# Kernel tuning notes

Measured on AMD Instinct MI355X. Metric: run time of the kernel, lower is better.

## Reference

```python
import jax, jax.numpy as jnp
import numpy as np

B, SQ, SK, D, H, F = 8, 512, 1024, 1024, 16, 4096
DK = D // H
NEG_INF = -jnp.inf


def _linear(x, w, b):
    return x @ w + b


def _mha(q, k, v, wq, bq, wk, bk, wv, bv, wo, bo, causal, kv_mask):
    # q: [B,Sq,D], k/v: [B,Sk,D]
    b, sq, d = q.shape
    sk = k.shape[1]
    Q = _linear(q, wq, bq).reshape(b, sq, H, DK).transpose(0, 2, 1, 3)  # [B,H,Sq,dk]
    K = _linear(k, wk, bk).reshape(b, sk, H, DK).transpose(0, 2, 1, 3)
    V = _linear(v, wv, bv).reshape(b, sk, H, DK).transpose(0, 2, 1, 3)
    S = jnp.einsum('bhqd,bhkd->bhqk', Q, K) / jnp.sqrt(jnp.asarray(DK, Q.dtype))
    if kv_mask is not None:
        S = jnp.where(kv_mask[:, None, None, :] == 0, NEG_INF, S)
    if causal:
        tri = jnp.tril(jnp.ones((sq, sk), dtype=bool))
        S = jnp.where(tri, S, NEG_INF)
    A = jax.nn.softmax(S, axis=-1)  # dropout p=0 -> identity
    x = jnp.einsum('bhqk,bhkd->bhqd', A, V).transpose(0, 2, 1, 3).reshape(b, sq, d)
    return _linear(x, wo, bo), A


def _ln(x, g, beta, eps=1e-5):
    mu = jnp.mean(x, axis=-1, keepdims=True)
    var = jnp.mean(jnp.square(x - mu), axis=-1, keepdims=True)
    return (x - mu) * jax.lax.rsqrt(var + eps) * g + beta


def setup_inputs() -> dict:
    key = jax.random.key(0)
    ks = jax.random.split(key, 32)
    s = 0.02
    inp = {
        'x': jax.random.normal(ks[0], (B, SQ, D), jnp.float32),
        'enc_o': jax.random.normal(ks[1], (B, SK, D), jnp.float32),
        'enc_mask': jax.random.randint(ks[2], (B, SK), 0, 2, jnp.int32),
    }
    i = 3
    for pfx in ('a1', 'a2'):
        for nm in ('wq', 'wk', 'wv', 'wo'):
            inp[f'{pfx}_{nm}'] = jax.random.normal(ks[i], (D, D), jnp.float32) * s; i += 1
            inp[f'{pfx}_{nm[1:] and "b" + nm[1:]}'] = jnp.zeros((D,), jnp.float32)
    inp['ff_w1'] = jax.random.normal(ks[i], (D, F), jnp.float32) * s; i += 1
    inp['ff_b1'] = jnp.zeros((F,), jnp.float32)
    inp['ff_w2'] = jax.random.normal(ks[i], (F, D), jnp.float32) * s; i += 1
    inp['ff_b2'] = jnp.zeros((D,), jnp.float32)
    for n in ('ln1', 'ln2', 'ln3'):
        inp[f'{n}_g'] = jnp.ones((D,), jnp.float32)
        inp[f'{n}_b'] = jnp.zeros((D,), jnp.float32)
    return inp


def reference(x, enc_o, enc_mask,
              a1_wq, a1_bq, a1_wk, a1_bk, a1_wv, a1_bv, a1_wo, a1_bo,
              a2_wq, a2_bq, a2_wk, a2_bk, a2_wv, a2_bv, a2_wo, a2_bo,
              ff_w1, ff_b1, ff_w2, ff_b2,
              ln1_g, ln1_b, ln2_g, ln2_b, ln3_g, ln3_b):
    res, _ = _mha(x, x, x, a1_wq, a1_bq, a1_wk, a1_bk, a1_wv, a1_bv, a1_wo, a1_bo,
                  causal=True, kv_mask=None)
    x = _ln(x + res, ln1_g, ln1_b)
    res, attn = _mha(x, enc_o, enc_o, a2_wq, a2_bq, a2_wk, a2_bk, a2_wv, a2_bv, a2_wo, a2_bo,
                     causal=False, kv_mask=enc_mask)
    x = _ln(x + res, ln2_g, ln2_b)
    res = _linear(jax.nn.relu(_linear(x, ff_w1, ff_b1)), ff_w2, ff_b2)
    x = _ln(x + res, ln3_g, ln3_b)
    return (x, attn)
```

## Files before the change

### kernel.cpp

```cpp
#include <hip/hip_runtime.h>
#include <hip/hip_bf16.h>


using bf16 = __hip_bfloat16;
typedef __attribute__((ext_vector_type(8))) short short8;
typedef __attribute__((ext_vector_type(4))) float f32x4;

#define DEVINL __device__ __forceinline__

DEVINL unsigned short bf16bits(float f) {
  __hip_bfloat16 h = __float2bfloat16(f);
  return *reinterpret_cast<unsigned short*>(&h);
}
DEVINL float bits2f(unsigned short u) {
  return __uint_as_float(((unsigned int)u) << 16);
}
DEVINL float tofloat(float f) { return f; }
DEVINL float tofloat(bf16 h) { return __bfloat162float(h); }

#define GLD16(gp, lp) __builtin_amdgcn_global_load_lds( \
    (__attribute__((address_space(1))) const void*)(gp), \
    (__attribute__((address_space(3))) void*)(lp), 16, 0, 0)

struct GemmP {
  const bf16* A; const bf16* Bt; void* C;
  const float* bias; const int* kmask;
  float scale;
  int M, N, K, lda, ldb, ldc;
  long sAb, sAh, sBb, sBh, sCb, sCh;
};

enum { EPI_BIAS_BF16 = 0, EPI_CAUSAL_BF16, EPI_KMASK_F32, EPI_NONE_BF16,
       EPI_BIAS_F32, EPI_BIAS_RELU_BF16, EPI_PART_F32 };

template<int EPI>
DEVINL void gemm_body(const GemmP& p, int bx, int by, int bz) {
  __shared__ bf16 As[128 * 32];
  __shared__ bf16 Bs[128 * 32];
  const int t = threadIdx.x;
  const int lane = t & 63;
  const int w = t >> 6;
  const int zb = bz >> 4, zh = bz & 15;
  const int m0 = by * 128, n0 = bx * 128;

  const bf16* Ab = p.A + (long)zb * p.sAb + (long)zh * p.sAh;
  const bf16* Bb = p.Bt + (long)zb * p.sBb + (long)zh * p.sBh;
  const int fl = lane & 15, fq = lane >> 4;
  const int wm = (w >> 1) * 64, wn = (w & 1) * 64;

  f32x4 acc[4][4];
#pragma unroll
  for (int i = 0; i < 4; ++i)
#pragma unroll
    for (int j = 0; j < 4; ++j) acc[i][j] = (f32x4){0.f, 0.f, 0.f, 0.f};

  const int sr = t >> 2;
  const int sc = (t & 3) * 8;
  char* ldsA = (char*)As + w * 1024;
  char* ldsB = (char*)Bs + w * 1024;

  int brow0 = n0 + sr;      if (brow0 > p.N - 1) brow0 = p.N - 1;
  int brow1 = n0 + sr + 64; if (brow1 > p.N - 1) brow1 = p.N - 1;

  for (int k0 = 0; k0 < p.K; k0 += 32) {
    GLD16(Ab + (long)(m0 + sr) * p.lda + k0 + sc, ldsA);
    GLD16(Ab + (long)(m0 + sr + 64) * p.lda + k0 + sc, ldsA + 4096);
    GLD16(Bb + (long)brow0 * p.ldb + k0 + sc, ldsB);
    GLD16(Bb + (long)brow1 * p.ldb + k0 + sc, ldsB + 4096);
    __syncthreads();

    short8 af[4], bfv[4];
#pragma unroll
    for (int i = 0; i < 4; ++i)
      af[i] = *(const short8*)(As + (wm + i * 16 + fl) * 32 + fq * 8);
#pragma unroll
    for (int j = 0; j < 4; ++j)
      bfv[j] = *(const short8*)(Bs + (wn + j * 16 + fl) * 32 + fq * 8);
#pragma unroll
    for (int i = 0; i < 4; ++i)
#pragma unroll
      for (int j = 0; j < 4; ++j)
        acc[i][j] = __builtin_amdgcn_mfma_f32_16x16x32_bf16(af[i], bfv[j], acc[i][j], 0, 0, 0);
    __syncthreads();
  }

  const float NEGINF = -__builtin_inff();
  const long cbase = (long)zb * p.sCb + (long)zh * p.sCh;
#pragma unroll
  for (int i = 0; i < 4; ++i) {
#pragma unroll
    for (int j = 0; j < 4; ++j) {
#pragma unroll
      for (int r = 0; r < 4; ++r) {
        int row = m0 + wm + i * 16 + fq * 4 + r;
        int col = n0 + wn + j * 16 + fl;
        if (col < p.N) {
          float v = acc[i][j][r];
          if (EPI == EPI_BIAS_BF16 || EPI == EPI_BIAS_F32 || EPI == EPI_BIAS_RELU_BF16)
            v += p.bias[col];
          if (EPI == EPI_BIAS_RELU_BF16) v = v > 0.f ? v : 0.f;
          if (EPI == EPI_CAUSAL_BF16) { v *= p.scale; if (col > row) v = NEGINF; }
          if (EPI == EPI_KMASK_F32)   { v *= p.scale; if (p.kmask[zb * 1024 + col] == 0) v = NEGINF; }
          long off = cbase + (long)row * p.ldc + col;
          if (EPI == EPI_KMASK_F32 || EPI == EPI_BIAS_F32 || EPI == EPI_PART_F32)
            ((float*)p.C)[off] = v;
          else ((bf16*)p.C)[off] = __float2bfloat16(v);
        }
      }
    }
  }
}

template<int EPI>
__global__ __launch_bounds__(256)
void gemm_k(GemmP p) {
  gemm_body<EPI>(p, blockIdx.x, blockIdx.y, blockIdx.z);
}

struct Gemm2P { GemmP a, b; int nA, axw, bxw; };
__global__ __launch_bounds__(256)
void gemm2_k(Gemm2P q) {
  const int b = blockIdx.x;
  if (b < q.nA) gemm_body<EPI_BIAS_BF16>(q.a, b % q.axw, b / q.axw, 0);
  else { const int c = b - q.nA; gemm_body<EPI_BIAS_BF16>(q.b, c % q.bxw, c / q.bxw, 0); }
}

struct AttnP {
  const bf16 *Q, *K, *Vt;
  float* Pout; bf16* O;
  const int* kmask;
  int ldq, ldk, ldv;
  long sQb, sQh, sKb, sKh, sVb, sVh, sPb, sPh, sOb, sOh;
};

template<int SK, bool CAUSAL, bool WRITE_P>
__global__ __launch_bounds__(512)
void attn_fused_k(AttnP p) {
  constexpr int TKMAX = SK / 64;
  __shared__ bf16 S[64 * SK];
  __shared__ bf16 ring[3 * 4096];
  const int t = threadIdx.x;
  const int lane = t & 63;
  const int w = t >> 6;
  const int fl = lane & 15, fq = lane >> 4;
  const int qh = w >> 2;
  const int wc = w & 3;
  const int lin = blockIdx.x;
  const int wg = (lin & 7) * 128 + (lin >> 3);
  const int by = wg & 7;
  const int z = wg >> 3;
  const int zb = z >> 4, zh = z & 15;
  const int q0 = by * 64;
  const float NEGINF = -__builtin_inff();

  const bf16* Qb = p.Q + (long)zb * p.sQb + (long)zh * p.sQh;
  const bf16* Kb = p.K + (long)zb * p.sKb + (long)zh * p.sKh;
  const bf16* Vb = p.Vt + (long)zb * p.sVb + (long)zh * p.sVh;

  const int Tk = CAUSAL ? (q0 >> 6) + 1 : TKMAX;

  short8 af[2][2];
#pragma unroll
  for (int i = 0; i < 2; ++i)
#pragma unroll
    for (int kk = 0; kk < 2; ++kk)
      af[i][kk] = *(const short8*)(Qb + (long)(q0 + qh * 32 + i * 16 + fl) * p.ldq + kk * 32 + fq * 8);

  int kmv[CAUSAL ? 1 : TKMAX];
  if (!CAUSAL) {
#pragma unroll
    for (int kt = 0; kt < TKMAX; ++kt)
      kmv[kt] = p.kmask[zb * 1024 + kt * 64 + wc * 16 + fl];
  }

  const int so = t * 16;
  const int srow = so >> 7;
  const int scb = (so & 127) ^ ((srow & 7) << 4);
  auto stage = [&](const bf16* mb, int ld, int roff, int coff, int buf) {
    GLD16(mb + (long)(roff + srow) * ld + coff + (scb >> 1),
          (char*)ring + buf * 8192 + w * 1024);
  };

  stage(Kb, p.ldk, 0, 0, 0);
  if (Tk > 1) stage(Kb, p.ldk, 64, 0, 1);
  for (int kt = 0; kt < Tk; ++kt) {
    if (kt + 1 < Tk) asm volatile("s_waitcnt vmcnt(1)" ::: "memory");
    else             asm volatile("s_waitcnt vmcnt(0)" ::: "memory");
    __builtin_amdgcn_s_barrier();
    if (kt + 2 < Tk) stage(Kb, p.ldk, (kt + 2) * 64, 0, (kt + 2) % 3);

    const char* kb = (const char*)ring + (kt % 3) * 8192;
    const int krow = wc * 16 + fl;
    short8 bfv[2];
#pragma unroll
    for (int kk = 0; kk < 2; ++kk)
      bfv[kk] = *(const short8*)(kb + ((krow * 128 + kk * 64 + fq * 16) ^ ((krow & 7) << 4)));
    f32x4 acc[2] = {(f32x4){0.f,0.f,0.f,0.f}, (f32x4){0.f,0.f,0.f,0.f}};
#pragma unroll
    for (int kk = 0; kk < 2; ++kk) {
      acc[0] = __builtin_amdgcn_mfma_f32_16x16x32_bf16(af[0][kk], bfv[kk], acc[0], 0, 0, 0);
      acc[1] = __builtin_amdgcn_mfma_f32_16x16x32_bf16(af[1][kk], bfv[kk], acc[1], 0, 0, 0);
    }
    const int col = kt * 64 + krow;
    const bool mok = CAUSAL || (kmv[CAUSAL ? 0 : kt] != 0);
#pragma unroll
    for (int i = 0; i < 2; ++i) {
#pragma unroll
      for (int r = 0; r < 4; ++r) {
        int row = qh * 32 + i * 16 + fq * 4 + r;
        float v = acc[i][r] * 0.125f;
        if (CAUSAL) { if (col > q0 + row) v = NEGINF; }
        else if (!mok) v = NEGINF;
        *(bf16*)((char*)S + (((row * SK + col) * 2) ^ ((row & 7) << 4))) = __float2bfloat16(v);
      }
    }
  }
  asm volatile("s_waitcnt lgkmcnt(0)" ::: "memory");
  __builtin_amdgcn_s_barrier();

  const int Tv = Tk;
  stage(Vb, p.ldv, 0, 0, 0);
  if (Tv > 1) stage(Vb, p.ldv, 0, 64, 1);

  float* Pf = WRITE_P ? (p.Pout + (long)zb * p.sPb + (long)zh * p.sPh) : nullptr;
  constexpr int NC = SK / 512;
  const int lim = Tk * 64;
  for (int rr = 0; rr < 8; ++rr) {
    const int row = w * 8 + rr;
    const int rg = q0 + row;
    const int swz = (row & 7) << 4;
    float fv[NC][8];
#pragma unroll
    for (int c = 0; c < NC; ++c) {
      const int col = c * 512 + lane * 8;
      if (!CAUSAL || col < lim) {
        short8 sv = *(const short8*)((char*)S + (((row * SK + col) * 2) ^ swz));
#pragma unroll
        for (int j = 0; j < 8; ++j) fv[c][j] = bits2f((unsigned short)sv[j]);
      } else {
#pragma unroll
        for (int j = 0; j < 8; ++j) fv[c][j] = NEGINF;
      }
    }
    float mx = fv[0][0];
#pragma unroll
    for (int c = 0; c < NC; ++c)
#pragma unroll
      for (int j = 0; j < 8; ++j) mx = fmaxf(mx, fv[c][j]);
    for (int off = 32; off; off >>= 1) mx = fmaxf(mx, __shfl_xor(mx, off, 64));
    float s = 0.f;
#pragma unroll
    for (int c = 0; c < NC; ++c)
#pragma unroll
      for (int j = 0; j < 8; ++j) { fv[c][j] = expf(fv[c][j] - mx); s += fv[c][j]; }
    for (int off = 32; off; off >>= 1) s += __shfl_xor(s, off, 64);
    const float inv = 1.f / s;
#pragma unroll
    for (int c = 0; c < NC; ++c) {
      const int col = c * 512 + lane * 8;
      if (!CAUSAL || col < lim) {
        short8 o;
#pragma unroll
        for (int j = 0; j < 8; ++j) o[j] = (short)bf16bits(fv[c][j] * inv);
        *(short8*)((char*)S + (((row * SK + col) * 2) ^ swz)) = o;
        if (WRITE_P) {
          float* pp = Pf + (long)rg * SK + col;
          f32x4 o0, o1;
#pragma unroll
          for (int j = 0; j < 4; ++j) { o0[j] = fv[c][j] * inv; o1[j] = fv[c][4 + j] * inv; }
          *(f32x4*)pp = o0;
          *(f32x4*)(pp + 4) = o1;
        }
      }
    }
  }
  asm volatile("s_waitcnt lgkmcnt(0)" ::: "memory");
  __builtin_amdgcn_s_barrier();

  f32x4 ao[2] = {(f32x4){0.f,0.f,0.f,0.f}, (f32x4){0.f,0.f,0.f,0.f}};
  for (int vt = 0; vt < Tv; ++vt) {
    if (vt + 1 < Tv) asm volatile("s_waitcnt vmcnt(1)" ::: "memory");
    else             asm volatile("s_waitcnt vmcnt(0)" ::: "memory");
    __builtin_amdgcn_s_barrier();
    if (vt + 2 < Tv) stage(Vb, p.ldv, 0, (vt + 2) * 64, (vt + 2) % 3);

    const char* vbuf = (const char*)ring + (vt % 3) * 8192;
    const int vrow = wc * 16 + fl;
    short8 bv[2];
#pragma unroll
    for (int kk = 0; kk < 2; ++kk)
      bv[kk] = *(const short8*)(vbuf + ((vrow * 128 + kk * 64 + fq * 16) ^ ((vrow & 7) << 4)));
#pragma unroll
    for (int i = 0; i < 2; ++i) {
      const int row = qh * 32 + i * 16 + fl;
#pragma unroll
      for (int kk = 0; kk < 2; ++kk) {
        const int col = vt * 64 + kk * 32 + fq * 8;
        short8 pa = *(const short8*)((char*)S + (((row * SK + col) * 2) ^ ((row & 7) << 4)));
        ao[i] = __builtin_amdgcn_mfma_f32_16x16x32_bf16(pa, bv[kk], ao[i], 0, 0, 0);
      }
    }
  }

  bf16* Ob_ = p.O + (long)zb * p.sOb + (long)zh * p.sOh;
#pragma unroll
  for (int i = 0; i < 2; ++i)
#pragma unroll
    for (int r = 0; r < 4; ++r) {
      int row = q0 + qh * 32 + i * 16 + fq * 4 + r;
      Ob_[(long)row * 1024 + wc * 16 + fl] = __float2bfloat16(ao[i][r]);
    }
}

template<int NP>
__global__ __launch_bounds__(256)
void ln_fuse_k(const float* __restrict__ x, const float* __restrict__ part, long pstride,
               const float* __restrict__ pb,
               const float* __restrict__ g, const float* __restrict__ bt,
               float* __restrict__ outf, bf16* __restrict__ outb) {
  const int lane = threadIdx.x & 63;
  const long row = (long)blockIdx.x * 4 + (threadIdx.x >> 6);
  const float* px = x + row * 1024;
  float4 v[4];
  float s = 0.f;
#pragma unroll
  for (int c = 0; c < 4; ++c) {
    const int col = c * 256 + lane * 4;
    float4 a = *(const float4*)(px + col);
    float4 bb = *(const float4*)(pb + col);
    v[c].x = a.x + bb.x; v[c].y = a.y + bb.y; v[c].z = a.z + bb.z; v[c].w = a.w + bb.w;
#pragma unroll
    for (int sl = 0; sl < NP; ++sl) {
      float4 pp = *(const float4*)(part + sl * pstride + row * 1024 + col);
      v[c].x += pp.x; v[c].y += pp.y; v[c].z += pp.z; v[c].w += pp.w;
    }
    s += v[c].x + v[c].y + v[c].z + v[c].w;
  }
  for (int off = 32; off; off >>= 1) s += __shfl_xor(s, off, 64);
  float mu = s * (1.f / 1024.f);
  float q = 0.f;
#pragma unroll
  for (int c = 0; c < 4; ++c) {
    float dx = v[c].x - mu, dy = v[c].y - mu, dz = v[c].z - mu, dw = v[c].w - mu;
    q += dx * dx + dy * dy + dz * dz + dw * dw;
  }
  for (int off = 32; off; off >>= 1) q += __shfl_xor(q, off, 64);
  float rs = rsqrtf(q * (1.f / 1024.f) + 1e-5f);
#pragma unroll
  for (int c = 0; c < 4; ++c) {
    int col = c * 256 + lane * 4;
    float4 gg = *(const float4*)(g + col);
    float4 bb = *(const float4*)(bt + col);
    float4 o;
    o.x = (v[c].x - mu) * rs * gg.x + bb.x;
    o.y = (v[c].y - mu) * rs * gg.y + bb.y;
    o.z = (v[c].z - mu) * rs * gg.z + bb.z;
    o.w = (v[c].w - mu) * rs * gg.w + bb.w;
    *(float4*)(outf + row * 1024 + col) = o;
    if (outb) {
      uint2 pk;
      pk.x = bf16bits(o.x) | ((unsigned)bf16bits(o.y) << 16);
      pk.y = bf16bits(o.z) | ((unsigned)bf16bits(o.w) << 16);
      *(uint2*)(outb + row * 1024 + col) = pk;
    }
  }
}

template<typename TI>
DEVINL void tr_body(const TI* __restrict__ pin, bf16* __restrict__ pout,
                    int ldi, int ldo, int c0, int r0, int t, float tile[32][33]) {
  const int tx = t & 31, ty = t >> 5;
#pragma unroll
  for (int i = 0; i < 32; i += 8)
    tile[ty + i][tx] = tofloat(pin[(long)(r0 + ty + i) * ldi + c0 + tx]);
  __syncthreads();
#pragma unroll
  for (int i = 0; i < 32; i += 8)
    pout[(long)(c0 + ty + i) * ldo + r0 + tx] = __float2bfloat16(tile[tx][ty + i]);
}

struct PrepP {
  const float *x, *enc;
  const float* wsrc[10];
  const float *b0, *b1, *b2, *b4, *b5;
  bf16 *xb, *encb, *wT;
  float *bqkv, *bkv;
};
__global__ __launch_bounds__(256)
void prep_k(PrepP p) {
  __shared__ float tile[32][33];
  const int b = blockIdx.x, t = threadIdx.x;
  if (b < 12288) {
    const float* src = (b < 4096) ? p.x : p.enc;
    bf16* dst = (b < 4096) ? p.xb : p.encb;
    long i = (long)(b < 4096 ? b : b - 4096) * 256 + t;
    float4 v = *(const float4*)(src + i * 4);
    uint2 pk;
    pk.x = bf16bits(v.x) | ((unsigned)bf16bits(v.y) << 16);
    pk.y = bf16bits(v.z) | ((unsigned)bf16bits(v.w) << 16);
    *(uint2*)(dst + i * 4) = pk;
  } else if (b < 20480) {
    int l = b - 12288; int wdx = l >> 10; l &= 1023;
    tr_body<float>(p.wsrc[wdx], p.wT + (long)wdx * 1048576, 1024, 1024,
                   (l & 31) * 32, (l >> 5) * 32, t, tile);
  } else if (b < 24576) {
    int l = b - 20480;
    tr_body<float>(p.wsrc[8], p.wT + 8l * 1048576, 4096, 1024,
                   (l & 127) * 32, (l >> 7) * 32, t, tile);
  } else if (b < 28672) {
    int l = b - 24576;
    tr_body<float>(p.wsrc[9], p.wT + 12l * 1048576, 1024, 4096,
                   (l % 32) * 32, (l / 32) * 32, t, tile);
  } else if (b < 28684) {
    int i = (b - 28672) * 256 + t;
    p.bqkv[i] = (i < 1024) ? p.b0[i] : (i < 2048 ? p.b1[i - 1024] : p.b2[i - 2048]);
  } else {
    int i = (b - 28684) * 256 + t;
    p.bkv[i] = (i < 1024) ? p.b4[i] : p.b5[i - 1024];
  }
}

struct Vt2P { const bf16 *vs, *vc; bf16 *vts, *vtc; };
__global__ __launch_bounds__(256)
void vt2_k(Vt2P p) {
  __shared__ float tile[32][33];
  const int b = blockIdx.x, t = threadIdx.x;
  if (b < 4096) {
    int z = b >> 5, l = b & 31;
    int zb = z >> 4, zh = z & 15;
    tr_body<bf16>(p.vs + (long)zb * 1572864 + zh * 64,
                  p.vts + (long)zb * 524288 + zh * 32768,
                  3072, 512, (l & 1) * 32, (l >> 1) * 32, t, tile);
  } else {
    int c = b - 4096;
    int z = c >> 6, l = c & 63;
    int zb = z >> 4, zh = z & 15;
    tr_body<bf16>(p.vc + (long)zb * 2097152 + zh * 64,
                  p.vtc + (long)zb * 1048576 + zh * 65536,
                  2048, 1024, (l & 1) * 32, (l >> 1) * 32, t, tile);
  }
}

static inline GemmP mkp(const void* A, const bf16* Bt, void* C,
                        const float* bias, const int* km, float sc,
                        int M, int N, int K, int lda, int ldb, int ldc,
                        long sAb, long sAh, long sBb, long sBh, long sCb, long sCh) {
  GemmP p;
  p.A = (const bf16*)A; p.Bt = Bt; p.C = C; p.bias = bias; p.kmask = km; p.scale = sc;
  p.M = M; p.N = N; p.K = K; p.lda = lda; p.ldb = ldb; p.ldc = ldc;
  p.sAb = sAb; p.sAh = sAh; p.sBb = sBb; p.sBh = sBh; p.sCb = sCb; p.sCh = sCh;
  return p;
}

extern "C" void kernel_launch(void* const* d_in, const int* in_sizes, int n_in,
                              void* d_out, int out_size, void* d_ws, size_t ws_size,
                              hipStream_t stream) {
  const float* x        = (const float*)d_in[0];
  const float* enc_o    = (const float*)d_in[1];
  const int*   enc_mask = (const int*)d_in[2];
  const float* a1_wq = (const float*)d_in[3];  const float* a1_bq = (const float*)d_in[4];
  const float* a1_wk = (const float*)d_in[5];  const float* a1_bk = (const float*)d_in[6];
  const float* a1_wv = (const float*)d_in[7];  const float* a1_bv = (const float*)d_in[8];
  const float* a1_wo = (const float*)d_in[9];  const float* a1_bo = (const float*)d_in[10];
  const float* a2_wq = (const float*)d_in[11]; const float* a2_bq = (const float*)d_in[12];
  const float* a2_wk = (const float*)d_in[13]; const float* a2_bk = (const float*)d_in[14];
  const float* a2_wv = (const float*)d_in[15]; const float* a2_bv = (const float*)d_in[16];
  const float* a2_wo = (const float*)d_in[17]; const float* a2_bo = (const float*)d_in[18];
  const float* ff_w1 = (const float*)d_in[19]; const float* ff_b1 = (const float*)d_in[20];
  const float* ff_w2 = (const float*)d_in[21]; const float* ff_b2 = (const float*)d_in[22];
  const float* ln1_g = (const float*)d_in[23]; const float* ln1_b = (const float*)d_in[24];
  const float* ln2_g = (const float*)d_in[25]; const float* ln2_b = (const float*)d_in[26];
  const float* ln3_g = (const float*)d_in[27]; const float* ln3_b = (const float*)d_in[28];

  const size_t MB = 1u << 20;
  const long M1 = 1048576;
  char* w = (char*)d_ws;
  bf16*  xb   = (bf16*)(w + 0);
  bf16*  encb = (bf16*)(w + 8 * MB);
  float* x1f  = (float*)(w + 24 * MB);
  float* x2f  = (float*)(w + 40 * MB);
  bf16*  xcb  = (bf16*)(w + 56 * MB);
  bf16*  wT   = (bf16*)(w + 64 * MB);
  float* bqkv = (float*)(w + 96 * MB);
  float* bkv  = (float*)(w + 96 * MB + 16384);
  bf16*  QKV  = (bf16*)(w + 104 * MB);
  bf16*  KVc  = (bf16*)(w + 128 * MB);
  bf16*  VtS  = (bf16*)(w + 160 * MB);
  bf16*  Ob   = (bf16*)(w + 176 * MB);
  float* part = (float*)(w + 200 * MB);
  bf16*  Asf  = (bf16*)(w + 264 * MB);
  bf16*  VtC  = (bf16*)(w + 332 * MB);

  float* out_x = (float*)d_out;
  float* attn  = (float*)d_out + 4194304;

  const dim3 blk(256);
  const dim3 blk5(512);

  {
    PrepP pp;
    pp.x = x; pp.enc = enc_o;
    pp.wsrc[0] = a1_wq; pp.wsrc[1] = a1_wk; pp.wsrc[2] = a1_wv; pp.wsrc[3] = a1_wo;
    pp.wsrc[4] = a2_wq; pp.wsrc[5] = a2_wk; pp.wsrc[6] = a2_wv; pp.wsrc[7] = a2_wo;
    pp.wsrc[8] = ff_w1; pp.wsrc[9] = ff_w2;
    pp.b0 = a1_bq; pp.b1 = a1_bk; pp.b2 = a1_bv; pp.b4 = a2_bk; pp.b5 = a2_bv;
    pp.xb = xb; pp.encb = encb; pp.wT = wT; pp.bqkv = bqkv; pp.bkv = bkv;
    prep_k<<<28692, blk, 0, stream>>>(pp);
  }

  {
    Gemm2P q;
    q.a = mkp(xb, wT, QKV, bqkv, nullptr, 0.f, 4096, 3072, 1024, 1024, 1024, 3072, 0,0,0,0,0,0);
    q.b = mkp(encb, wT + 5 * M1, KVc, bkv, nullptr, 0.f, 8192, 2048, 1024, 1024, 1024, 2048, 0,0,0,0,0,0);
    q.nA = 768; q.axw = 24; q.bxw = 16;
    gemm2_k<<<1792, blk, 0, stream>>>(q);
  }
  bf16* Qs = QKV;
  bf16* Ks = QKV + 1024;
  bf16* Vs = QKV + 2048;
  bf16* Kc = KVc;
  bf16* Vc = KVc + 1024;

  {
    Vt2P vp; vp.vs = Vs; vp.vc = Vc; vp.vts = VtS; vp.vtc = VtC;
    vt2_k<<<12288, blk, 0, stream>>>(vp);
  }

  {
    AttnP ap;
    ap.Q = Qs; ap.K = Ks; ap.Vt = VtS; ap.Pout = nullptr; ap.O = Ob; ap.kmask = nullptr;
    ap.ldq = 3072; ap.ldk = 3072; ap.ldv = 512;
    ap.sQb = 1572864; ap.sQh = 64; ap.sKb = 1572864; ap.sKh = 64;
    ap.sVb = 524288;  ap.sVh = 32768; ap.sPb = 0; ap.sPh = 0;
    ap.sOb = 524288;  ap.sOh = 64;
    attn_fused_k<512, true, false><<<dim3(1024), blk5, 0, stream>>>(ap);
  }

  gemm_k<EPI_PART_F32><<<dim3(8, 32, 2), blk, 0, stream>>>(
      mkp(Ob, wT + 3 * M1, part, nullptr, nullptr, 0.f, 4096, 1024, 512, 1024, 1024, 1024,
          0, 512, 0, 512, 0, 4194304));

  ln_fuse_k<2><<<1024, blk, 0, stream>>>(x, part, 4194304, a1_bo, ln1_g, ln1_b, x1f, xcb);

  gemm_k<EPI_BIAS_BF16><<<dim3(8, 32, 1), blk, 0, stream>>>(
      mkp(xcb, wT + 4 * M1, QKV, a2_bq, nullptr, 0.f, 4096, 1024, 1024, 1024, 1024, 1024, 0,0,0,0,0,0));
  bf16* Qc = QKV;

  {
    AttnP ap;
    ap.Q = Qc; ap.K = Kc; ap.Vt = VtC; ap.Pout = attn; ap.O = Ob; ap.kmask = enc_mask;
    ap.ldq = 1024; ap.ldk = 2048; ap.ldv = 1024;
    ap.sQb = 524288;  ap.sQh = 64; ap.sKb = 2097152; ap.sKh = 64;
    ap.sVb = 1048576; ap.sVh = 65536; ap.sPb = 8388608; ap.sPh = 524288;
    ap.sOb = 524288;  ap.sOh = 64;
    attn_fused_k<1024, false, true><<<dim3(1024), blk5, 0, stream>>>(ap);
  }

  gemm_k<EPI_PART_F32><<<dim3(8, 32, 2), blk, 0, stream>>>(
      mkp(Ob, wT + 7 * M1, part, nullptr, nullptr, 0.f, 4096, 1024, 512, 1024, 1024, 1024,
          0, 512, 0, 512, 0, 4194304));

  ln_fuse_k<2><<<1024, blk, 0, stream>>>(x1f, part, 4194304, a2_bo, ln2_g, ln2_b, x2f, xcb);

  gemm_k<EPI_BIAS_RELU_BF16><<<dim3(32, 32, 1), blk, 0, stream>>>(
      mkp(xcb, wT + 8 * M1, Asf, ff_b1, nullptr, 0.f, 4096, 4096, 1024, 1024, 1024, 4096, 0,0,0,0,0,0));

  gemm_k<EPI_PART_F32><<<dim3(8, 32, 4), blk, 0, stream>>>(
      mkp(Asf, wT + 12 * M1, part, nullptr, nullptr, 0.f, 4096, 1024, 1024, 4096, 4096, 1024,
          0, 1024, 0, 1024, 0, 4194304));

  ln_fuse_k<4><<<1024, blk, 0, stream>>>(x2f, part, 4194304, ff_b2, ln3_g, ln3_b, out_x, nullptr);
}
```

Before: 988.2 us.

## Load K/V fragments directly into registers instead of LDS ring staging

Removes the triple-buffered LDS ring that used async global-to-LDS loads with barriers for K and V tiles. Each wave now loads its own K/V MFMA fragments straight from global memory into registers, prefetching one tile ahead. This drops per-tile block barriers and LDS traffic, and frees 24KB of shared memory, which may help occupancy. In exchange, the two waves that share each K/V slice (qh=0 and 1) each fetch it, so global and L2 reads double, and the loads are less coalesced than the staged copies.

```diff
diff --git a/kernel.cpp b/kernel.cpp
--- a/kernel.cpp
+++ b/kernel.cpp
@@ -138,7 +138,6 @@
 void attn_fused_k(AttnP p) {
   constexpr int TKMAX = SK / 64;
   __shared__ bf16 S[64 * SK];
-  __shared__ bf16 ring[3 * 4096];
   const int t = threadIdx.x;
   const int lane = t & 63;
   const int w = t >> 6;
@@ -173,35 +172,25 @@
       kmv[kt] = p.kmask[zb * 1024 + kt * 64 + wc * 16 + fl];
   }
 
-  const int so = t * 16;
-  const int srow = so >> 7;
-  const int scb = (so & 127) ^ ((srow & 7) << 4);
-  auto stage = [&](const bf16* mb, int ld, int roff, int coff, int buf) {
-    GLD16(mb + (long)(roff + srow) * ld + coff + (scb >> 1),
-          (char*)ring + buf * 8192 + w * 1024);
-  };
-
-  stage(Kb, p.ldk, 0, 0, 0);
-  if (Tk > 1) stage(Kb, p.ldk, 64, 0, 1);
+  const bf16* kbase = Kb + (long)(wc * 16 + fl) * p.ldk + fq * 8;
+  const long kstep = (long)64 * p.ldk;
+  short8 kcur[2];
+  kcur[0] = *(const short8*)(kbase);
+  kcur[1] = *(const short8*)(kbase + 32);
   for (int kt = 0; kt < Tk; ++kt) {
-    if (kt + 1 < Tk) asm volatile("s_waitcnt vmcnt(1)" ::: "memory");
-    else             asm volatile("s_waitcnt vmcnt(0)" ::: "memory");
-    __builtin_amdgcn_s_barrier();
-    if (kt + 2 < Tk) stage(Kb, p.ldk, (kt + 2) * 64, 0, (kt + 2) % 3);
-
-    const char* kb = (const char*)ring + (kt % 3) * 8192;
-    const int krow = wc * 16 + fl;
-    short8 bfv[2];
-#pragma unroll
-    for (int kk = 0; kk < 2; ++kk)
-      bfv[kk] = *(const short8*)(kb + ((krow * 128 + kk * 64 + fq * 16) ^ ((krow & 7) << 4)));
+    short8 knxt[2];
+    if (kt + 1 < Tk) {
+      const bf16* kp = kbase + (long)(kt + 1) * kstep;
+      knxt[0] = *(const short8*)(kp);
+      knxt[1] = *(const short8*)(kp + 32);
+    }
     f32x4 acc[2] = {(f32x4){0.f,0.f,0.f,0.f}, (f32x4){0.f,0.f,0.f,0.f}};
 #pragma unroll
     for (int kk = 0; kk < 2; ++kk) {
-      acc[0] = __builtin_amdgcn_mfma_f32_16x16x32_bf16(af[0][kk], bfv[kk], acc[0], 0, 0, 0);
-      acc[1] = __builtin_amdgcn_mfma_f32_16x16x32_bf16(af[1][kk], bfv[kk], acc[1], 0, 0, 0);
-    }
-    const int col = kt * 64 + krow;
+      acc[0] = __builtin_amdgcn_mfma_f32_16x16x32_bf16(af[0][kk], kcur[kk], acc[0], 0, 0, 0);
+      acc[1] = __builtin_amdgcn_mfma_f32_16x16x32_bf16(af[1][kk], kcur[kk], acc[1], 0, 0, 0);
+    }
+    const int col = kt * 64 + wc * 16 + fl;
     const bool mok = CAUSAL || (kmv[CAUSAL ? 0 : kt] != 0);
 #pragma unroll
     for (int i = 0; i < 2; ++i) {
@@ -214,13 +203,9 @@
         *(bf16*)((char*)S + (((row * SK + col) * 2) ^ ((row & 7) << 4))) = __float2bfloat16(v);
       }
     }
-  }
-  asm volatile("s_waitcnt lgkmcnt(0)" ::: "memory");
-  __builtin_amdgcn_s_barrier();
-
-  const int Tv = Tk;
-  stage(Vb, p.ldv, 0, 0, 0);
-  if (Tv > 1) stage(Vb, p.ldv, 0, 64, 1);
+    kcur[0] = knxt[0]; kcur[1] = knxt[1];
+  }
+  __syncthreads();
 
   float* Pf = WRITE_P ? (p.Pout + (long)zb * p.sPb + (long)zh * p.sPh) : nullptr;
   constexpr int NC = SK / 512;
@@ -274,22 +259,20 @@
       }
     }
   }
-  asm volatile("s_waitcnt lgkmcnt(0)" ::: "memory");
-  __builtin_amdgcn_s_barrier();
-
+  __syncthreads();
+
+  const bf16* vbase = Vb + (long)(wc * 16 + fl) * p.ldv + fq * 8;
   f32x4 ao[2] = {(f32x4){0.f,0.f,0.f,0.f}, (f32x4){0.f,0.f,0.f,0.f}};
-  for (int vt = 0; vt < Tv; ++vt) {
-    if (vt + 1 < Tv) asm volatile("s_waitcnt vmcnt(1)" ::: "memory");
-    else             asm volatile("s_waitcnt vmcnt(0)" ::: "memory");
-    __builtin_amdgcn_s_barrier();
-    if (vt + 2 < Tv) stage(Vb, p.ldv, 0, (vt + 2) * 64, (vt + 2) % 3);
-
-    const char* vbuf = (const char*)ring + (vt % 3) * 8192;
-    const int vrow = wc * 16 + fl;
-    short8 bv[2];
-#pragma unroll
-    for (int kk = 0; kk < 2; ++kk)
-      bv[kk] = *(const short8*)(vbuf + ((vrow * 128 + kk * 64 + fq * 16) ^ ((vrow & 7) << 4)));
+  short8 vcur[2];
+  vcur[0] = *(const short8*)(vbase);
+  vcur[1] = *(const short8*)(vbase + 32);
+  for (int vt = 0; vt < Tk; ++vt) {
+    short8 vnxt[2];
+    if (vt + 1 < Tk) {
+      const bf16* vp = vbase + (vt + 1) * 64;
+      vnxt[0] = *(const short8*)(vp);
+      vnxt[1] = *(const short8*)(vp + 32);
+    }
 #pragma unroll
     for (int i = 0; i < 2; ++i) {
       const int row = qh * 32 + i * 16 + fl;
@@ -297,9 +280,10 @@
       for (int kk = 0; kk < 2; ++kk) {
         const int col = vt * 64 + kk * 32 + fq * 8;
         short8 pa = *(const short8*)((char*)S + (((row * SK + col) * 2) ^ ((row & 7) << 4)));
-        ao[i] = __builtin_amdgcn_mfma_f32_16x16x32_bf16(pa, bv[kk], ao[i], 0, 0, 0);
+        ao[i] = __builtin_amdgcn_mfma_f32_16x16x32_bf16(pa, vcur[kk], ao[i], 0, 0, 0);
       }
     }
+    vcur[0] = vnxt[0]; vcur[1] = vnxt[1];
   }
 
   bf16* Ob_ = p.O + (long)zb * p.sOb + (long)zh * p.sOh;
```

Result: faster. 953.9 us (-3.5%).
